# Kernel optimization log

Measured on AMD Instinct MI355X. Metric: run time of the kernel, lower is better.

Reference implementation:

```python
import jax, jax.numpy as jnp
import numpy as np

NGRAM = 16
SUB = 512  # bytes per sub-block


def byte2image(block, ngram=NGRAM):
    """block: (B, L) int -> (B, 1, ngram*8, L-ngram) float32 in [-1, 1]."""
    B, L = block.shape
    blk = block.astype(jnp.int32)
    # nxt[:, i] = blk[:, i+1], last column zero
    nxt = jnp.concatenate([blk[:, 1:], jnp.zeros((B, 1), jnp.int32)], axis=1)
    # 8 bit-shifted views of the byte stream
    shifts = jnp.stack(
        [((blk << s) & 255) + ((nxt >> (8 - s)) & 255) for s in range(8)],
        axis=1,
    )  # (B, 8, L)
    flat = shifts.reshape(B, -1)  # (B, 8*L)
    parts = [flat] + [jnp.roll(flat, -i, axis=1) for i in range(1, ngram)]
    stacked = jnp.concatenate(parts, axis=1).reshape(B, ngram * 8, L)
    result = stacked[:, :, :-ngram].astype(jnp.float32)
    result = (result / 255.0 - 0.5) / 0.5
    return result[:, None]  # (B, 1, ngram*8, L-ngram)


def byte2image_4k(block, ngram=NGRAM):
    """block: (B, 4096) -> (B, 8, ngram*8, 512-ngram)."""
    return jnp.concatenate(
        [byte2image(block[:, i * SUB:(i + 1) * SUB], ngram) for i in range(8)],
        axis=1,
    )


def setup_inputs() -> dict:
    key = jax.random.key(0)
    kx, kw = jax.random.split(key)
    x = jax.random.randint(kx, (256, 4096), 0, 256, dtype=jnp.int64)
    W = jax.random.normal(kw, (496, 64), dtype=jnp.float32) * 0.02
    return {"x": x, "W": W}


def reference(x, W):
    # ByteFormerWrapper.forward with block_size=4096: byte2image_4k then the
    # (opaque) model; model stood in by a linear head over the image width.
    img = byte2image_4k(x)                      # (B, 8, 128, 496)
    out = jnp.einsum('bchw,wo->bcho', img, W)   # (B, 8, 128, 64)
    return out
```

## Files before the change

kernel.cpp:

```cpp
#include <hip/hip_runtime.h>

typedef unsigned short u16;
typedef unsigned int u32;
typedef __attribute__((ext_vector_type(8))) short short8;
typedef _Float16 half8 __attribute__((ext_vector_type(8)));
typedef __attribute__((ext_vector_type(4))) float floatx4;

#define LSTRIDE 72

__global__ __launch_bounds__(256, 4) void byteformer_fused(
    const int* __restrict__ x, const float* __restrict__ Wm,
    float* __restrict__ out) {
  __shared__ __align__(16) u16 As[128 * LSTRIDE];
  __shared__ __align__(16) u16 Bs[128 * LSTRIDE];
  __shared__ float part[256];
  __shared__ float csum[64];

  const int t = threadIdx.x;
  const int mtile = blockIdx.x;
  const int n0 = blockIdx.y * 128;
  const int p0 = 2 * blockIdx.y;

  const int wave = t >> 6, lane = t & 63;
  const int wm = wave >> 1, wn = wave & 1;
  const int quad = lane >> 4, l16 = lane & 15;

  const int sA_sub = t >> 4;
  const int sA_kg  = (t >> 1) & 7;
  const int sA_qh  = t & 1;
  const long xrow = ((long)mtile * 16 + sA_sub) * 512;

  const int sB_o = lane;

  floatx4 acc[4][4];
  #pragma unroll
  for (int mt = 0; mt < 4; ++mt)
    #pragma unroll
    for (int nt = 0; nt < 4; ++nt)
      acc[mt][nt] = floatx4{0.f, 0.f, 0.f, 0.f};

  float csum_local = 0.0f;

  for (int kc = 0; kc < 8; ++kc) {
    const int k0 = kc * 64;
    __syncthreads();

    {
      const int base = k0 + sA_kg * 8;
      int4 a0 = *(const int4*)&x[xrow + base];
      int4 a1 = *(const int4*)&x[xrow + base + 4];
      int c8 = (base + 8 < 512) ? x[xrow + base + 8] : 0;
      int c[9] = {a0.x, a0.y, a0.z, a0.w, a1.x, a1.y, a1.z, a1.w, c8};
      u32 w16[8];
      #pragma unroll
      for (int j = 0; j < 8; ++j) w16[j] = ((u32)c[j] << 8) | (u32)c[j + 1];
      #pragma unroll
      for (int qi = 0; qi < 4; ++qi) {
        const int q = sA_qh * 4 + qi;
        const int sh = 8 - q;
        u32 d[4];
        #pragma unroll
        for (int jp = 0; jp < 4; ++jp) {
          u32 v0 = (w16[2 * jp] >> sh) & 255u;
          u32 v1 = (w16[2 * jp + 1] >> sh) & 255u;
          d[jp] = v0 | (v1 << 16) | 0x64006400u;
        }
        *(u32*)&As[(sA_sub * 8 + q) * LSTRIDE + sA_kg * 8 + 0] = d[0];
        *(u32*)&As[(sA_sub * 8 + q) * LSTRIDE + sA_kg * 8 + 2] = d[1];
        *(u32*)&As[(sA_sub * 8 + q) * LSTRIDE + sA_kg * 8 + 4] = d[2];
        *(u32*)&As[(sA_sub * 8 + q) * LSTRIDE + sA_kg * 8 + 6] = d[3];
      }
    }

    {
      const int cbase = k0 + 16 * wave - p0 - 1;
      float f[17];
      u16 h[17];
      #pragma unroll
      for (int j = 0; j < 17; ++j) {
        int c = cbase + j;
        float v = (c >= 0 && c < 496) ? Wm[c * 64 + sB_o] : 0.0f;
        f[j] = v;
        h[j] = (u16)__builtin_bit_cast(unsigned short, (_Float16)v);
      }
      #pragma unroll
      for (int j = 1; j <= 16; ++j) csum_local += f[j];
      #pragma unroll
      for (int g = 0; g < 2; ++g) {
        const int mgrp = 2 * wave + g;
        #pragma unroll
        for (int pp = 0; pp < 2; ++pp) {
          const int jb = g * 8 + 1 - pp;
          u32 d[4];
          #pragma unroll
          for (int di = 0; di < 4; ++di)
            d[di] = (u32)h[jb + 2 * di] | ((u32)h[jb + 2 * di + 1] << 16);
          u32* dst = (u32*)&Bs[(pp * 64 + sB_o) * LSTRIDE + mgrp * 8];
          dst[0] = d[0]; dst[1] = d[1]; dst[2] = d[2]; dst[3] = d[3];
        }
      }
    }
    __syncthreads();

    #pragma unroll
    for (int ks = 0; ks < 2; ++ks) {
      const int koff = ks * 32 + quad * 8;
      half8 af[4], bf[4];
      #pragma unroll
      for (int mt = 0; mt < 4; ++mt)
        af[mt] = *(const half8*)&As[(wm * 64 + mt * 16 + l16) * LSTRIDE + koff];
      #pragma unroll
      for (int nt = 0; nt < 4; ++nt)
        bf[nt] = *(const half8*)&Bs[(wn * 64 + nt * 16 + l16) * LSTRIDE + koff];
      #pragma unroll
      for (int mt = 0; mt < 4; ++mt)
        #pragma unroll
        for (int nt = 0; nt < 4; ++nt)
          acc[mt][nt] = __builtin_amdgcn_mfma_f32_16x16x32_f16(
              af[mt], bf[nt], acc[mt][nt], 0, 0, 0);
    }
  }

  part[t] = csum_local;
  __syncthreads();
  if (t < 64)
    csum[t] = part[t] + part[t + 64] + part[t + 128] + part[t + 192];
  __syncthreads();

  const float S = 2.0f / 255.0f;
  const float K1 = 1024.0f * S + 1.0f;
  #pragma unroll
  for (int nt = 0; nt < 4; ++nt) {
    int n = n0 + wn * 64 + nt * 16 + l16;
    int p = n >> 6, o = n & 63;
    float cs = K1 * csum[o];
    #pragma unroll
    for (int mt = 0; mt < 4; ++mt) {
      int mbase = mtile * 128 + wm * 64 + mt * 16 + quad * 4;
      #pragma unroll
      for (int i = 0; i < 4; ++i) {
        int mr = mbase + i;
        int bid = mr >> 3, q = mr & 7;
        out[(long)bid * 8192 + (p * 8 + q) * 64 + o] = S * acc[mt][nt][i] - cs;
      }
    }
  }
}

extern "C" void kernel_launch(void* const* d_in, const int* in_sizes, int n_in,
                              void* d_out, int out_size, void* d_ws, size_t ws_size,
                              hipStream_t stream) {
  const int* x = (const int*)d_in[0];
  const float* Wm = (const float*)d_in[1];
  float* out = (float*)d_out;
  byteformer_fused<<<dim3(128, 8), dim3(256), 0, stream>>>(x, Wm, out);
}
```

Baseline: 104.1 us.

## Precompute fp16 B tiles in a prologue kernel and stream them via global_load_lds

A small prologue kernel now converts W into padded fp16 LDS-layout tiles (64 images) and computes the column-sum bias once, writing both to workspace. The main kernel copies B tiles straight into LDS with global_load_lds instead of reconverting W in every block, and prefetches the next x chunk into registers after the barrier. The A-tile bit-shift packing is also simplified to packed 32-bit ops with int4 stores. This removes the redundant per-block W conversion and reduction, at the cost of an extra kernel launch and workspace traffic.

```diff
diff --git a/kernel.cpp b/kernel.cpp
--- a/kernel.cpp
+++ b/kernel.cpp
@@ -2,24 +2,67 @@
 
 typedef unsigned short u16;
 typedef unsigned int u32;
-typedef __attribute__((ext_vector_type(8))) short short8;
 typedef _Float16 half8 __attribute__((ext_vector_type(8)));
 typedef __attribute__((ext_vector_type(4))) float floatx4;
 
 #define LSTRIDE 72
+#define BIMG (128 * LSTRIDE)
+
+__device__ __forceinline__ void gl_lds16(const void* g, void* l) {
+  __builtin_amdgcn_global_load_lds(
+      (const __attribute__((address_space(1))) void*)g,
+      (__attribute__((address_space(3))) void*)l, 16, 0, 0);
+}
+__device__ __forceinline__ void gl_lds4(const void* g, void* l) {
+  __builtin_amdgcn_global_load_lds(
+      (const __attribute__((address_space(1))) void*)g,
+      (__attribute__((address_space(3))) void*)l, 4, 0, 0);
+}
+
+__global__ __launch_bounds__(256) void byteformer_precompute(
+    const float* __restrict__ Wm, u16* __restrict__ Bws,
+    float* __restrict__ csumWs) {
+  const int t = threadIdx.x;
+  const int y = blockIdx.x >> 3, kc = blockIdx.x & 7;
+  const int wave = t >> 6, o = t & 63;
+  const int pp = wave >> 1, hf = wave & 1;
+  u16* img = Bws + (size_t)blockIdx.x * BIMG;
+  #pragma unroll
+  for (int i = 0; i < 18; ++i) {
+    const int kk = (hf * 18 + i) * 2;
+    u32 val = 0u;
+    if (kk < 64) {
+      const int c0 = kc * 64 + kk - 2 * y - pp;
+      const int c1 = c0 + 1;
+      float f0 = (c0 >= 0 && c0 < 496) ? Wm[c0 * 64 + o] : 0.0f;
+      float f1 = (c1 >= 0 && c1 < 496) ? Wm[c1 * 64 + o] : 0.0f;
+      u16 h0 = __builtin_bit_cast(unsigned short, (_Float16)f0);
+      u16 h1 = __builtin_bit_cast(unsigned short, (_Float16)f1);
+      val = (u32)h0 | ((u32)h1 << 16);
+    }
+    *(u32*)&img[(pp * 64 + o) * LSTRIDE + kk] = val;
+  }
+  if (blockIdx.x == 0) {
+    __shared__ float red[256];
+    float s = 0.0f;
+    for (int c = wave * 124; c < wave * 124 + 124; ++c) s += Wm[c * 64 + o];
+    red[t] = s;
+    __syncthreads();
+    if (t < 64)
+      csumWs[t] = (1024.0f * (2.0f / 255.0f) + 1.0f) *
+                  (red[t] + red[t + 64] + red[t + 128] + red[t + 192]);
+  }
+}
 
 __global__ __launch_bounds__(256, 4) void byteformer_fused(
-    const int* __restrict__ x, const float* __restrict__ Wm,
-    float* __restrict__ out) {
+    const int* __restrict__ x, const u16* __restrict__ Bws,
+    const float* __restrict__ csumWs, float* __restrict__ out) {
   __shared__ __align__(16) u16 As[128 * LSTRIDE];
   __shared__ __align__(16) u16 Bs[128 * LSTRIDE];
-  __shared__ float part[256];
-  __shared__ float csum[64];
 
   const int t = threadIdx.x;
   const int mtile = blockIdx.x;
   const int n0 = blockIdx.y * 128;
-  const int p0 = 2 * blockIdx.y;
 
   const int wave = t >> 6, lane = t & 63;
   const int wm = wave >> 1, wn = wave & 1;
@@ -30,7 +73,7 @@
   const int sA_qh  = t & 1;
   const long xrow = ((long)mtile * 16 + sA_sub) * 512;
 
-  const int sB_o = lane;
+  const char* bimg0 = (const char*)(Bws + (size_t)blockIdx.y * 8 * BIMG);
 
   floatx4 acc[4][4];
   #pragma unroll
@@ -39,68 +82,59 @@
     for (int nt = 0; nt < 4; ++nt)
       acc[mt][nt] = floatx4{0.f, 0.f, 0.f, 0.f};
 
-  float csum_local = 0.0f;
+  int4 ca, cb; int cc;
+  {
+    const int base = sA_kg * 8;
+    ca = *(const int4*)&x[xrow + base];
+    cb = *(const int4*)&x[xrow + base + 4];
+    cc = x[xrow + base + 8];
+  }
 
   for (int kc = 0; kc < 8; ++kc) {
-    const int k0 = kc * 64;
     __syncthreads();
 
     {
-      const int base = k0 + sA_kg * 8;
-      int4 a0 = *(const int4*)&x[xrow + base];
-      int4 a1 = *(const int4*)&x[xrow + base + 4];
-      int c8 = (base + 8 < 512) ? x[xrow + base + 8] : 0;
-      int c[9] = {a0.x, a0.y, a0.z, a0.w, a1.x, a1.y, a1.z, a1.w, c8};
-      u32 w16[8];
+      const char* src = bimg0 + (size_t)kc * (BIMG * 2);
+      char* dst = (char*)Bs;
+      const int woff = wave * 1024;
       #pragma unroll
-      for (int j = 0; j < 8; ++j) w16[j] = ((u32)c[j] << 8) | (u32)c[j + 1];
+      for (int j = 0; j < 4; ++j)
+        gl_lds16(src + j * 4096 + woff + lane * 16, dst + j * 4096 + woff);
+      const int woff4 = 16384 + wave * 256;
+      #pragma unroll
+      for (int j = 0; j < 2; ++j)
+        gl_lds4(src + woff4 + j * 1024 + lane * 4, dst + woff4 + j * 1024);
+    }
+
+    {
+      const u32 c0 = (u32)ca.x, c1 = (u32)ca.y, c2 = (u32)ca.z, c3 = (u32)ca.w;
+      const u32 c4 = (u32)cb.x, c5 = (u32)cb.y, c6 = (u32)cb.z, c7 = (u32)cb.w;
+      const u32 c8 = (u32)cc;
+      const u32 P0 = ((c0 << 8) | c1) | (((c1 << 8) | c2) << 16);
+      const u32 P1 = ((c2 << 8) | c3) | (((c3 << 8) | c4) << 16);
+      const u32 P2 = ((c4 << 8) | c5) | (((c5 << 8) | c6) << 16);
+      const u32 P3 = ((c6 << 8) | c7) | (((c7 << 8) | c8) << 16);
+      u16* arow = &As[(sA_sub * 8 + sA_qh * 4) * LSTRIDE + sA_kg * 8];
       #pragma unroll
       for (int qi = 0; qi < 4; ++qi) {
-        const int q = sA_qh * 4 + qi;
-        const int sh = 8 - q;
-        u32 d[4];
-        #pragma unroll
-        for (int jp = 0; jp < 4; ++jp) {
-          u32 v0 = (w16[2 * jp] >> sh) & 255u;
-          u32 v1 = (w16[2 * jp + 1] >> sh) & 255u;
-          d[jp] = v0 | (v1 << 16) | 0x64006400u;
-        }
-        *(u32*)&As[(sA_sub * 8 + q) * LSTRIDE + sA_kg * 8 + 0] = d[0];
-        *(u32*)&As[(sA_sub * 8 + q) * LSTRIDE + sA_kg * 8 + 2] = d[1];
-        *(u32*)&As[(sA_sub * 8 + q) * LSTRIDE + sA_kg * 8 + 4] = d[2];
-        *(u32*)&As[(sA_sub * 8 + q) * LSTRIDE + sA_kg * 8 + 6] = d[3];
+        const int sh = 8 - (sA_qh * 4 + qi);
+        int4 d;
+        d.x = (int)(((P0 >> sh) & 0x00FF00FFu) | 0x64006400u);
+        d.y = (int)(((P1 >> sh) & 0x00FF00FFu) | 0x64006400u);
+        d.z = (int)(((P2 >> sh) & 0x00FF00FFu) | 0x64006400u);
+        d.w = (int)(((P3 >> sh) & 0x00FF00FFu) | 0x64006400u);
+        *(int4*)(arow + qi * LSTRIDE) = d;
       }
     }
 
-    {
-      const int cbase = k0 + 16 * wave - p0 - 1;
-      float f[17];
-      u16 h[17];
-      #pragma unroll
-      for (int j = 0; j < 17; ++j) {
-        int c = cbase + j;
-        float v = (c >= 0 && c < 496) ? Wm[c * 64 + sB_o] : 0.0f;
-        f[j] = v;
-        h[j] = (u16)__builtin_bit_cast(unsigned short, (_Float16)v);
-      }
-      #pragma unroll
-      for (int j = 1; j <= 16; ++j) csum_local += f[j];
-      #pragma unroll
-      for (int g = 0; g < 2; ++g) {
-        const int mgrp = 2 * wave + g;
-        #pragma unroll
-        for (int pp = 0; pp < 2; ++pp) {
-          const int jb = g * 8 + 1 - pp;
-          u32 d[4];
-          #pragma unroll
-          for (int di = 0; di < 4; ++di)
-            d[di] = (u32)h[jb + 2 * di] | ((u32)h[jb + 2 * di + 1] << 16);
-          u32* dst = (u32*)&Bs[(pp * 64 + sB_o) * LSTRIDE + mgrp * 8];
-          dst[0] = d[0]; dst[1] = d[1]; dst[2] = d[2]; dst[3] = d[3];
-        }
-      }
+    __syncthreads();
+
+    if (kc < 7) {
+      const int base = (kc + 1) * 64 + sA_kg * 8;
+      ca = *(const int4*)&x[xrow + base];
+      cb = *(const int4*)&x[xrow + base + 4];
+      cc = (base + 8 < 512) ? x[xrow + base + 8] : 0;
     }
-    __syncthreads();
 
     #pragma unroll
     for (int ks = 0; ks < 2; ++ks) {
@@ -121,27 +155,20 @@
     }
   }
 
-  part[t] = csum_local;
-  __syncthreads();
-  if (t < 64)
-    csum[t] = part[t] + part[t + 64] + part[t + 128] + part[t + 192];
-  __syncthreads();
-
   const float S = 2.0f / 255.0f;
-  const float K1 = 1024.0f * S + 1.0f;
   #pragma unroll
   for (int nt = 0; nt < 4; ++nt) {
     int n = n0 + wn * 64 + nt * 16 + l16;
     int p = n >> 6, o = n & 63;
-    float cs = K1 * csum[o];
+    float cs = csumWs[o];
     #pragma unroll
     for (int mt = 0; mt < 4; ++mt) {
       int mbase = mtile * 128 + wm * 64 + mt * 16 + quad * 4;
       #pragma unroll
       for (int i = 0; i < 4; ++i) {
         int mr = mbase + i;
-        int bid = mr >> 3, q = mr & 7;
-        out[(long)bid * 8192 + (p * 8 + q) * 64 + o] = S * acc[mt][nt][i] - cs;
+        int sub = mr >> 3, q = mr & 7;
+        out[(long)sub * 8192 + (p * 8 + q) * 64 + o] = S * acc[mt][nt][i] - cs;
       }
     }
   }
@@ -153,5 +180,8 @@
   const int* x = (const int*)d_in[0];
   const float* Wm = (const float*)d_in[1];
   float* out = (float*)d_out;
-  byteformer_fused<<<dim3(128, 8), dim3(256), 0, stream>>>(x, Wm, out);
+  u16* Bws = (u16*)d_ws;
+  float* csumWs = (float*)((char*)d_ws + (size_t)64 * BIMG * 2);
+  byteformer_precompute<<<dim3(64), dim3(256), 0, stream>>>(Wm, Bws, csumWs);
+  byteformer_fused<<<dim3(128, 8), dim3(256), 0, stream>>>(x, Bws, csumWs, out);
 }
```

New measurement: 117.6 us. +13.0%, slower.
